# Kernel optimization log

Hardware: AMD Instinct MI355X
Metric: run time of the kernel (lower is better)

Reference implementation:

```python
import jax, jax.numpy as jnp
import numpy as np

N = 192            # image grid size (NxN)
N_SHOTS = 192
N_SAMPLES = 192
TWO_PI = 2.0 * np.pi
PIPE_ITERS = 3     # gpunufft default is ~10; 3 suffices for a CPU-runnable reference


def initialize_2D_radial(n_shots, n_samples):
    """Radial trajectory, k in [-0.5, 0.5), shape (n_shots*n_samples, 2)."""
    angles = np.pi * np.arange(n_shots) / n_shots
    radii = np.linspace(-0.5, 0.5, n_samples, endpoint=False)
    kx = radii[None, :] * np.cos(angles[:, None])
    ky = radii[None, :] * np.sin(angles[:, None])
    return np.stack([kx, ky], axis=-1).reshape(-1, 2).astype(np.float32)


def setup_inputs() -> dict:
    key = jax.random.key(0)
    x = jax.random.normal(key, (2, N, N), dtype=jnp.float32)  # real/imag image
    trajectory = jnp.asarray(initialize_2D_radial(N_SHOTS, N_SAMPLES))  # (M,2)
    return {"x": x, "trajectory": trajectory}


def _mats(traj):
    # Separable NDFT factors: exp(-2pi i k_x * px), exp(-2pi i k_y * py).
    # A: (M, N), B: (M, N); M*N complex64 ~= 57 MB each.
    p = jnp.arange(N, dtype=jnp.float32) - N / 2.0  # centered pixel coords
    A = jnp.exp(-1j * TWO_PI * traj[:, 0:1] * p[None, :])
    B = jnp.exp(-1j * TWO_PI * traj[:, 1:2] * p[None, :])
    return A.astype(jnp.complex64), B.astype(jnp.complex64)


def _op(img, A, B):
    # type-2 NUFFT (exact NDFT): image (N,N) -> kspace (M,)
    t = jnp.einsum('my,xy->mx', B, img)      # contract y first
    return jnp.einsum('mx,mx->m', A, t)


def _adj(d, A, B):
    # type-1 NUFFT adjoint: samples (M,) -> image (N,N)
    return jnp.einsum('mx,my->xy', jnp.conj(A) * d[:, None], jnp.conj(B))


def _pipe_density(A, B):
    # Pipe & Menon iterative density compensation: w <- w / |F F^H w|
    w = jnp.ones(A.shape[0], dtype=jnp.complex64)
    def body(i, w):
        q = _op(_adj(w, A, B), A, B)
        return w / jnp.maximum(jnp.abs(q), 1e-20)
    w = jax.lax.fori_loop(0, PIPE_ITERS, body, w)
    return jnp.abs(w)  # real positive weights


def reference(x, trajectory):
    img = (x[0] + 1j * x[1]).astype(jnp.complex64)  # (N,N) complex image
    A, B = _mats(trajectory)
    # density weights computed from detached trajectory (gpunufft init-time)
    traj_sg = jax.lax.stop_gradient(trajectory)
    Asg, Bsg = _mats(traj_sg)
    w = jax.lax.stop_gradient(_pipe_density(Asg, Bsg))
    kspace = _op(img, A, B)                       # forward NUFFT
    adjoint = _adj(w * kspace, A, B)              # density-compensated adjoint
    return jnp.stack([adjoint.real, adjoint.imag])  # (2,N,N) float32
```

## Files before the change

### kernel.cpp

```cpp
#include <hip/hip_runtime.h>
#include <math.h>


#define MTOT 36864
#define NPIX 192
#define SPLITS 128
#define MPS (MTOT / SPLITS)
#define ADJ_CHUNKS (MPS / 16)
#define PG 4

typedef __attribute__((ext_vector_type(8))) short s16x8;
typedef __attribute__((ext_vector_type(4))) float f32x4;
typedef __attribute__((ext_vector_type(4))) unsigned u32x4;

__device__ __forceinline__ f32x4 mfma_bf16(u32x4 a, u32x4 b, f32x4 c) {
    return __builtin_amdgcn_mfma_f32_16x16x32_bf16(
        __builtin_bit_cast(s16x8, a), __builtin_bit_cast(s16x8, b), c, 0, 0, 0);
}

__device__ __forceinline__ void g2l16(const void* g, void* l) {
    __builtin_amdgcn_global_load_lds(
        (const __attribute__((address_space(1))) void*)g,
        (__attribute__((address_space(3))) void*)l, 16, 0, 0);
}

__device__ __forceinline__ void split_pk(float a, float b, unsigned &hi, unsigned &lo) {
    const unsigned ua = __float_as_uint(a), ub = __float_as_uint(b);
    const unsigned ha = (ua + 0x8000u) & 0xffff0000u;
    const unsigned hb = (ub + 0x8000u) & 0xffff0000u;
    hi = (ha >> 16) | hb;
    const float la = a - __uint_as_float(ha);
    const float lb = b - __uint_as_float(hb);
    lo = ((__float_as_uint(la) + 0x8000u) >> 16) |
         ((__float_as_uint(lb) + 0x8000u) & 0xffff0000u);
}

__device__ __forceinline__ void ksplit(float k, float &kh, float &kl) {
    kh = __uint_as_float(__float_as_uint(k) & 0xfffff000u);
    kl = k - kh;
}
__device__ __forceinline__ float redphase(float kh, float kl, float p) {
    float r = kh * p;
    r -= rintf(r);
    r = fmaf(kl, p, r);
    return r;
}
__device__ __forceinline__ unsigned rot16(unsigned v) {
    return __builtin_amdgcn_alignbit(v, v, 16);
}
__device__ __forceinline__ int swz(int c) {
    return ((c ^ (c >> 2)) & 3) << 2;
}

__global__ void precompP_k(const float* __restrict__ traj, const int comp,
                           unsigned* __restrict__ PS) {
    const int m = blockIdx.x * 256 + threadIdx.x;
    const int c = blockIdx.y;
    float kh, kl; ksplit(traj[2 * m + comp], kh, kl);
    const float ph = redphase(kh, kl, (float)(c - 96));
    const float co = __builtin_amdgcn_cosf(ph);
    const float si = __builtin_amdgcn_sinf(ph);
    unsigned h, l; split_pk(co, -si, h, l);
    const int mc = m >> 4, mi = (m & 15) ^ swz(c);
    PS[(size_t)mc * 6144 + c * 16 + mi]        = h;
    PS[(size_t)mc * 6144 + 3072 + c * 16 + mi] = l;
}

__global__ void ebuild_k(const float* __restrict__ traj,
                         const float* __restrict__ dr, const float* __restrict__ di,
                         unsigned* __restrict__ ES) {
    const int m = blockIdx.x * 256 + threadIdx.x;
    const int c = blockIdx.y;
    float kh, kl; ksplit(traj[2 * m], kh, kl);
    const float ph = redphase(kh, kl, (float)(c - 96));
    const float co = __builtin_amdgcn_cosf(ph);
    const float si = __builtin_amdgcn_sinf(ph);
    const float dr_ = dr[m], di_ = di[m];
    const float Er = co * dr_ - si * di_;
    const float Ei = co * di_ + si * dr_;
    unsigned h, l; split_pk(Er, Ei, h, l);
    const int mc = m >> 4, mi = (m & 15) ^ swz(c);
    ES[(size_t)mc * 6144 + c * 16 + mi]        = h;
    ES[(size_t)mc * 6144 + 3072 + c * 16 + mi] = l;
}

__global__ void winit_k(float* __restrict__ wr, float* __restrict__ wi) {
    const int m = blockIdx.x * 256 + threadIdx.x;
    wr[m] = 1.f; wi[m] = 0.f;
}

__global__ __launch_bounds__(256) void adj_gemm_k(
    const unsigned* __restrict__ ES, const unsigned* __restrict__ BS,
    float* __restrict__ outP)
{
    __shared__ unsigned sAB[3][4096];
    const int tid = threadIdx.x;
    const int lane = tid & 63, wid = tid >> 6;
    const int l15 = lane & 15, qd = lane >> 4;
    const int L = blockIdx.x;
    const int xcd = L & 7, j = L >> 3;
    const int s = xcd * (SPLITS / 8) + j / 9;
    const int tile = j % 9;
    const int bx = tile % 3, by = tile / 3;
    const int wi = wid & 1, wj = wid >> 1;
    const int x0 = bx * 64 + wi * 32, y0 = by * 64 + wj * 32;
    float* outRe = outP + (size_t)(s & (PG - 1)) * (2 * MTOT);
    float* outIm = outRe + MTOT;

    f32x4 accRe[2][2], accIm[2][2];
    #pragma unroll
    for (int i = 0; i < 2; ++i)
        #pragma unroll
        for (int j2 = 0; j2 < 2; ++j2) {
            accRe[i][j2] = (f32x4){0.f, 0.f, 0.f, 0.f};
            accIm[i][j2] = (f32x4){0.f, 0.f, 0.f, 0.f};
        }

    const unsigned* gp[4];
    {
        const unsigned* E0 = ES + (size_t)(s * ADJ_CHUNKS) * 6144;
        const unsigned* B0 = BS + (size_t)(s * ADJ_CHUNKS) * 6144;
        gp[0] = E0 + bx * 1024 + tid * 4;
        gp[1] = E0 + 3072 + bx * 1024 + tid * 4;
        gp[2] = B0 + by * 1024 + tid * 4;
        gp[3] = B0 + 3072 + by * 1024 + tid * 4;
    }
    int eoff[2], boff[2];
    #pragma unroll
    for (int t = 0; t < 2; ++t) {
        const int cE = wi * 32 + t * 16 + l15;
        eoff[t] = cE * 16 + ((qd ^ ((cE ^ (cE >> 2)) & 3)) << 2);
        const int cB = wj * 32 + t * 16 + l15;
        boff[t] = 2048 + cB * 16 + ((qd ^ ((cB ^ (cB >> 2)) & 3)) << 2);
    }

    #pragma unroll
    for (int v = 0; v < 4; ++v)
        g2l16(gp[v], &sAB[0][v * 1024 + tid * 4]);
    #pragma unroll
    for (int v = 0; v < 4; ++v) {
        gp[v] += 6144;
        g2l16(gp[v], &sAB[1][v * 1024 + tid * 4]);
    }

    int rb = 0;
    for (int ch = 0; ch < ADJ_CHUNKS; ++ch) {
        if (ch + 2 < ADJ_CHUNKS) {
            const int wb = (rb + 2 >= 3) ? rb - 1 : rb + 2;
            #pragma unroll
            for (int v = 0; v < 4; ++v) {
                gp[v] += 6144;
                g2l16(gp[v], &sAB[wb][v * 1024 + tid * 4]);
            }
            asm volatile("s_waitcnt vmcnt(8)" ::: "memory");
        } else if (ch + 1 < ADJ_CHUNKS) {
            asm volatile("s_waitcnt vmcnt(4)" ::: "memory");
        } else {
            asm volatile("s_waitcnt vmcnt(0)" ::: "memory");
        }
        __builtin_amdgcn_s_barrier();

        const unsigned* sb = &sAB[rb][0];
        u32x4 Eh[2], El[2], PhA[2], PlA[2];
        #pragma unroll
        for (int t = 0; t < 2; ++t) {
            Eh[t]  = *(const u32x4*)(sb + eoff[t]);
            El[t]  = *(const u32x4*)(sb + 1024 + eoff[t]);
            PhA[t] = *(const u32x4*)(sb + boff[t]);
            PlA[t] = *(const u32x4*)(sb + 1024 + boff[t]);
        }
        asm volatile("s_waitcnt lgkmcnt(0)" ::: "memory");
        __builtin_amdgcn_sched_barrier(0);
        __builtin_amdgcn_s_barrier();

        #pragma unroll
        for (int sj = 0; sj < 2; ++sj) {
            const u32x4 Ph = PhA[sj], Pl = PlA[sj];
            u32x4 Qh, Ql;
            #pragma unroll
            for (int r = 0; r < 4; ++r) {
                Qh[r] = rot16(Ph[r]) ^ 0x00008000u;
                Ql[r] = rot16(Pl[r]) ^ 0x00008000u;
            }
            #pragma unroll
            for (int si = 0; si < 2; ++si) {
                accRe[si][sj] = mfma_bf16(Eh[si], Ph, accRe[si][sj]);
                accRe[si][sj] = mfma_bf16(Eh[si], Pl, accRe[si][sj]);
                accRe[si][sj] = mfma_bf16(El[si], Ph, accRe[si][sj]);
                accIm[si][sj] = mfma_bf16(Eh[si], Qh, accIm[si][sj]);
                accIm[si][sj] = mfma_bf16(Eh[si], Ql, accIm[si][sj]);
                accIm[si][sj] = mfma_bf16(El[si], Qh, accIm[si][sj]);
            }
        }
        rb = (rb + 1 == 3) ? 0 : rb + 1;
    }

    #pragma unroll
    for (int si = 0; si < 2; ++si)
        #pragma unroll
        for (int sj = 0; sj < 2; ++sj)
            #pragma unroll
            for (int rg = 0; rg < 4; ++rg) {
                const int x = x0 + si * 16 + qd * 4 + rg;
                const int y = y0 + sj * 16 + l15;
                atomicAdd(outRe + x * NPIX + y, accRe[si][sj][rg]);
                atomicAdd(outIm + x * NPIX + y, accIm[si][sj][rg]);
            }
}

__device__ __forceinline__ void fw_stage_load(const unsigned* __restrict__ Ghi,
                                              const unsigned* __restrict__ Glo,
                                              int tid, int koff, u32x4 st[3]) {
    #pragma unroll
    for (int j = 0; j < 3; ++j) {
        const int li = tid + j * 576;
        if (li < 1536) {
            const int row = li >> 3, pl = (li >> 2) & 1, qt = li & 3;
            const unsigned* src = pl ? Glo : Ghi;
            st[j] = *(const u32x4*)(src + row * 192 + koff + qt * 4);
        }
    }
}
__device__ __forceinline__ void fw_stage_write(unsigned* sb, int tid, const u32x4 st[3]) {
    #pragma unroll
    for (int j = 0; j < 3; ++j) {
        const int li = tid + j * 576;
        if (li < 1536) {
            const int row = li >> 3, pl = (li >> 2) & 1, qt = li & 3;
            *(u32x4*)(sb + pl * 3840 + row * 20 + qt * 4) = st[j];
        }
    }
}

__global__ __launch_bounds__(576) void fwdq_k(
    const float* __restrict__ traj,
    const unsigned* __restrict__ Ghi, const unsigned* __restrict__ Glo,
    float* __restrict__ wre, float* __restrict__ wim,
    const int mode,
    float* __restrict__ qre, float* __restrict__ qim)
{
    __shared__ unsigned sG[2][2 * 3840];
    const int tid = threadIdx.x;
    const int lane = tid & 63, wid = tid >> 6;
    const int l15 = lane & 15, q = lane >> 4;
    const int m = (blockIdx.x * 9 + wid) * 16 + l15;
    const float2 kk = *(const float2*)(traj + 2 * m);
    float kxh, kxl, kyh, kyl;
    ksplit(kk.x, kxh, kxl);
    ksplit(kk.y, kyh, kyl);

    f32x4 tre[12], tim[12];
    #pragma unroll
    for (int i = 0; i < 12; ++i) {
        tre[i] = (f32x4){0.f, 0.f, 0.f, 0.f};
        tim[i] = (f32x4){0.f, 0.f, 0.f, 0.f};
    }

    float bc, bs;
    { const float ph = redphase(kyh, kyl, (float)(q * 4 - 96)); 
      bc = __builtin_amdgcn_cosf(ph); bs = __builtin_amdgcn_sinf(ph); }
    const float r1c = __builtin_amdgcn_cosf(kk.y), r1s = __builtin_amdgcn_sinf(kk.y);
    float r16c, r16s;
    { float g = kk.y * 16.f; g -= rintf(g);
      r16c = __builtin_amdgcn_cosf(g); r16s = __builtin_amdgcn_sinf(g); }

    u32x4 st[3];
    fw_stage_load(Ghi, Glo, tid, 0, st);
    fw_stage_write(&sG[0][0], tid, st);
    __syncthreads();

    for (int ch = 0; ch < 12; ++ch) {
        if (ch < 11) fw_stage_load(Ghi, Glo, tid, (ch + 1) * 16, st);

        u32x4 Ph, Pl, Qh, Ql;
        {
            float c = bc, s = bs;
            #pragma unroll
            for (int r = 0; r < 4; ++r) {
                unsigned h, l; split_pk(c, s, h, l);
                Ph[r] = h; Pl[r] = l;
                Qh[r] = rot16(h) ^ 0x00008000u;
                Ql[r] = rot16(l) ^ 0x00008000u;
                const float nc = c * r1c - s * r1s, ns = s * r1c + c * r1s;
                c = nc; s = ns;
            }
            const float nbc = bc * r16c - bs * r16s, nbs = bs * r16c + bc * r16s;
            bc = nbc; bs = nbs;
        }

        const unsigned* sb = &sG[ch & 1][0];
        #pragma unroll
        for (int si = 0; si < 12; ++si) {
            const int base = (si * 16 + l15) * 20 + q * 4;
            const u32x4 gh = *(const u32x4*)(sb + base);
            const u32x4 gl = *(const u32x4*)(sb + 3840 + base);
            tre[si] = mfma_bf16(gh, Ph, tre[si]);
            tre[si] = mfma_bf16(gh, Pl, tre[si]);
            tre[si] = mfma_bf16(gl, Ph, tre[si]);
            tim[si] = mfma_bf16(gh, Qh, tim[si]);
            tim[si] = mfma_bf16(gh, Ql, tim[si]);
            tim[si] = mfma_bf16(gl, Qh, tim[si]);
        }

        if (ch < 11) {
            __syncthreads();
            fw_stage_write(&sG[(ch + 1) & 1][0], tid, st);
            __syncthreads();
        }
    }

    float qr = 0.f, qi = 0.f;
    {
        float g = kk.x * 16.f; g -= rintf(g);
        const float rc = __builtin_amdgcn_cosf(g), rs = __builtin_amdgcn_sinf(g);
        #pragma unroll
        for (int rg = 0; rg < 4; ++rg) {
            const float ph = redphase(kxh, kxl, (float)(q * 4 + rg - 96));
            float c = __builtin_amdgcn_cosf(ph), s = __builtin_amdgcn_sinf(ph);
            #pragma unroll
            for (int si = 0; si < 12; ++si) {
                const float tr = tre[si][rg], ti = tim[si][rg];
                qr += c * tr + s * ti;
                qi += c * ti - s * tr;
                const float nc = c * rc - s * rs, ns = s * rc + c * rs;
                c = nc; s = ns;
            }
        }
    }
    qr += __shfl_xor(qr, 16); qi += __shfl_xor(qi, 16);
    qr += __shfl_xor(qr, 32); qi += __shfl_xor(qi, 32);
    if (lane < 16) {
        if (mode == 0) {
            const float den = fmaxf(sqrtf(qr * qr + qi * qi), 1e-20f);
            wre[m] /= den; wim[m] /= den;
        } else {
            const float sc = sqrtf(wre[m] * wre[m] + wim[m] * wim[m]);
            qre[m] = qr * sc; qim[m] = qi * sc;
        }
    }
}

__global__ void presplit_k(const float* __restrict__ re, const float* __restrict__ im,
                           unsigned* __restrict__ Gh, unsigned* __restrict__ Gl) {
    const int e = blockIdx.x * 256 + threadIdx.x;
    unsigned h, l;
    split_pk(re[e], im[e], h, l);
    Gh[e] = h; Gl[e] = l;
}

__global__ void presplitP_k(const float* __restrict__ outP,
                            unsigned* __restrict__ Gh, unsigned* __restrict__ Gl) {
    const int e = blockIdx.x * 256 + threadIdx.x;
    float re = 0.f, im = 0.f;
    #pragma unroll
    for (int g = 0; g < PG; ++g) {
        re += outP[(size_t)g * (2 * MTOT) + e];
        im += outP[(size_t)g * (2 * MTOT) + MTOT + e];
    }
    unsigned h, l;
    split_pk(re, im, h, l);
    Gh[e] = h; Gl[e] = l;
}

__global__ void reduceOut_k(const float* __restrict__ outP, float* __restrict__ out) {
    const int e = blockIdx.x * 256 + threadIdx.x;
    float re = 0.f, im = 0.f;
    #pragma unroll
    for (int g = 0; g < PG; ++g) {
        re += outP[(size_t)g * (2 * MTOT) + e];
        im += outP[(size_t)g * (2 * MTOT) + MTOT + e];
    }
    out[e] = re; out[MTOT + e] = im;
}

extern "C" void kernel_launch(void* const* d_in, const int* in_sizes, int n_in,
                              void* d_out, int out_size, void* d_ws, size_t ws_size,
                              hipStream_t stream)
{
    const float* xin  = (const float*)d_in[0];
    const float* traj = (const float*)d_in[1];
    float* out = (float*)d_out;

    char* pb = (char*)d_ws;
    unsigned* BS = (unsigned*)pb; pb += (size_t)2304 * 6144 * 4;
    unsigned* ES = (unsigned*)pb; pb += (size_t)2304 * 6144 * 4;
    float* outP = (float*)pb; pb += (size_t)PG * 2 * MTOT * 4;
    float* wr   = (float*)pb; pb += MTOT * 4;
    float* wi   = (float*)pb; pb += MTOT * 4;
    float* dre  = (float*)pb; pb += MTOT * 4;
    float* dim_ = (float*)pb; pb += MTOT * 4;
    unsigned* Ghi = (unsigned*)pb; pb += MTOT * 4;
    unsigned* Glo = (unsigned*)pb; pb += MTOT * 4;

    precompP_k<<<dim3(MTOT / 256, NPIX), 256, 0, stream>>>(traj, 1, BS);
    winit_k<<<MTOT / 256, 256, 0, stream>>>(wr, wi);

    for (int it = 0; it < 3; ++it) {
        hipMemsetAsync(outP, 0, (size_t)PG * 2 * MTOT * 4, stream);
        ebuild_k<<<dim3(MTOT / 256, NPIX), 256, 0, stream>>>(traj, wr, wi, ES);
        adj_gemm_k<<<9 * SPLITS, 256, 0, stream>>>(ES, BS, outP);
        presplitP_k<<<MTOT / 256, 256, 0, stream>>>(outP, Ghi, Glo);
        fwdq_k<<<256, 576, 0, stream>>>(traj, Ghi, Glo, wr, wi, 0, dre, dim_);
    }

    presplit_k<<<MTOT / 256, 256, 0, stream>>>(xin, xin + MTOT, Ghi, Glo);
    fwdq_k<<<256, 576, 0, stream>>>(traj, Ghi, Glo, wr, wi, 1, dre, dim_);
    hipMemsetAsync(outP, 0, (size_t)PG * 2 * MTOT * 4, stream);
    ebuild_k<<<dim3(MTOT / 256, NPIX), 256, 0, stream>>>(traj, dre, dim_, ES);
    adj_gemm_k<<<9 * SPLITS, 256, 0, stream>>>(ES, BS, outP);
    reduceOut_k<<<MTOT / 256, 256, 0, stream>>>(outP, out);
}
```

Measured before the change: 497.9 us.

## Replace atomic split-K accumulation with per-group partial planes and drop memsets

```diff
diff --git a/kernel.cpp b/kernel.cpp
--- a/kernel.cpp
+++ b/kernel.cpp
@@ -5,9 +5,9 @@
 #define MTOT 36864
 #define NPIX 192
 #define SPLITS 128
-#define MPS (MTOT / SPLITS)
-#define ADJ_CHUNKS (MPS / 16)
-#define PG 4
+#define GRP 64
+#define NCH 36
+#define PG 64
 
 typedef __attribute__((ext_vector_type(8))) short s16x8;
 typedef __attribute__((ext_vector_type(4))) float f32x4;
@@ -99,12 +99,12 @@
     const int l15 = lane & 15, qd = lane >> 4;
     const int L = blockIdx.x;
     const int xcd = L & 7, j = L >> 3;
-    const int s = xcd * (SPLITS / 8) + j / 9;
+    const int g = xcd * (GRP / 8) + j / 9;
     const int tile = j % 9;
     const int bx = tile % 3, by = tile / 3;
     const int wi = wid & 1, wj = wid >> 1;
     const int x0 = bx * 64 + wi * 32, y0 = by * 64 + wj * 32;
-    float* outRe = outP + (size_t)(s & (PG - 1)) * (2 * MTOT);
+    float* outRe = outP + (size_t)g * (2 * MTOT);
     float* outIm = outRe + MTOT;
 
     f32x4 accRe[2][2], accIm[2][2];
@@ -116,15 +116,20 @@
             accIm[i][j2] = (f32x4){0.f, 0.f, 0.f, 0.f};
         }
 
-    const unsigned* gp[4];
-    {
-        const unsigned* E0 = ES + (size_t)(s * ADJ_CHUNKS) * 6144;
-        const unsigned* B0 = BS + (size_t)(s * ADJ_CHUNKS) * 6144;
-        gp[0] = E0 + bx * 1024 + tid * 4;
-        gp[1] = E0 + 3072 + bx * 1024 + tid * 4;
-        gp[2] = B0 + by * 1024 + tid * 4;
-        gp[3] = B0 + 3072 + by * 1024 + tid * 4;
-    }
+    const size_t g18 = (size_t)g * 18;
+    const int exo = bx * 1024 + tid * 4;
+    const int byo = by * 1024 + tid * 4;
+    #define STAGE(c, buf)                                                  \
+    {                                                                      \
+        const size_t id_ = (g18 + (c) + (((c) >= 18) ? 1134 : 0)) * 6144; \
+        const unsigned* E0_ = ES + id_;                                    \
+        const unsigned* B0_ = BS + id_;                                    \
+        g2l16(E0_ + exo,        &sAB[buf][tid * 4]);                       \
+        g2l16(E0_ + 3072 + exo, &sAB[buf][1024 + tid * 4]);                \
+        g2l16(B0_ + byo,        &sAB[buf][2048 + tid * 4]);                \
+        g2l16(B0_ + 3072 + byo, &sAB[buf][3072 + tid * 4]);                \
+    }
+
     int eoff[2], boff[2];
     #pragma unroll
     for (int t = 0; t < 2; ++t) {
@@ -134,26 +139,16 @@
         boff[t] = 2048 + cB * 16 + ((qd ^ ((cB ^ (cB >> 2)) & 3)) << 2);
     }
 
-    #pragma unroll
-    for (int v = 0; v < 4; ++v)
-        g2l16(gp[v], &sAB[0][v * 1024 + tid * 4]);
-    #pragma unroll
-    for (int v = 0; v < 4; ++v) {
-        gp[v] += 6144;
-        g2l16(gp[v], &sAB[1][v * 1024 + tid * 4]);
-    }
+    STAGE(0, 0);
+    STAGE(1, 1);
 
     int rb = 0;
-    for (int ch = 0; ch < ADJ_CHUNKS; ++ch) {
-        if (ch + 2 < ADJ_CHUNKS) {
+    for (int ch = 0; ch < NCH; ++ch) {
+        if (ch + 2 < NCH) {
             const int wb = (rb + 2 >= 3) ? rb - 1 : rb + 2;
-            #pragma unroll
-            for (int v = 0; v < 4; ++v) {
-                gp[v] += 6144;
-                g2l16(gp[v], &sAB[wb][v * 1024 + tid * 4]);
-            }
+            STAGE(ch + 2, wb);
             asm volatile("s_waitcnt vmcnt(8)" ::: "memory");
-        } else if (ch + 1 < ADJ_CHUNKS) {
+        } else if (ch + 1 < NCH) {
             asm volatile("s_waitcnt vmcnt(4)" ::: "memory");
         } else {
             asm volatile("s_waitcnt vmcnt(0)" ::: "memory");
@@ -194,6 +189,7 @@
         }
         rb = (rb + 1 == 3) ? 0 : rb + 1;
     }
+    #undef STAGE
 
     #pragma unroll
     for (int si = 0; si < 2; ++si)
@@ -203,8 +199,8 @@
             for (int rg = 0; rg < 4; ++rg) {
                 const int x = x0 + si * 16 + qd * 4 + rg;
                 const int y = y0 + sj * 16 + l15;
-                atomicAdd(outRe + x * NPIX + y, accRe[si][sj][rg]);
-                atomicAdd(outIm + x * NPIX + y, accIm[si][sj][rg]);
+                outRe[x * NPIX + y] = accRe[si][sj][rg];
+                outIm[x * NPIX + y] = accIm[si][sj][rg];
             }
 }
 
@@ -352,7 +348,7 @@
                             unsigned* __restrict__ Gh, unsigned* __restrict__ Gl) {
     const int e = blockIdx.x * 256 + threadIdx.x;
     float re = 0.f, im = 0.f;
-    #pragma unroll
+    #pragma unroll 8
     for (int g = 0; g < PG; ++g) {
         re += outP[(size_t)g * (2 * MTOT) + e];
         im += outP[(size_t)g * (2 * MTOT) + MTOT + e];
@@ -365,7 +361,7 @@
 __global__ void reduceOut_k(const float* __restrict__ outP, float* __restrict__ out) {
     const int e = blockIdx.x * 256 + threadIdx.x;
     float re = 0.f, im = 0.f;
-    #pragma unroll
+    #pragma unroll 8
     for (int g = 0; g < PG; ++g) {
         re += outP[(size_t)g * (2 * MTOT) + e];
         im += outP[(size_t)g * (2 * MTOT) + MTOT + e];
@@ -396,17 +392,15 @@
     winit_k<<<MTOT / 256, 256, 0, stream>>>(wr, wi);
 
     for (int it = 0; it < 3; ++it) {
-        hipMemsetAsync(outP, 0, (size_t)PG * 2 * MTOT * 4, stream);
         ebuild_k<<<dim3(MTOT / 256, NPIX), 256, 0, stream>>>(traj, wr, wi, ES);
-        adj_gemm_k<<<9 * SPLITS, 256, 0, stream>>>(ES, BS, outP);
+        adj_gemm_k<<<9 * GRP, 256, 0, stream>>>(ES, BS, outP);
         presplitP_k<<<MTOT / 256, 256, 0, stream>>>(outP, Ghi, Glo);
         fwdq_k<<<256, 576, 0, stream>>>(traj, Ghi, Glo, wr, wi, 0, dre, dim_);
     }
 
     presplit_k<<<MTOT / 256, 256, 0, stream>>>(xin, xin + MTOT, Ghi, Glo);
     fwdq_k<<<256, 576, 0, stream>>>(traj, Ghi, Glo, wr, wi, 1, dre, dim_);
-    hipMemsetAsync(outP, 0, (size_t)PG * 2 * MTOT * 4, stream);
     ebuild_k<<<dim3(MTOT / 256, NPIX), 256, 0, stream>>>(traj, dre, dim_, ES);
-    adj_gemm_k<<<9 * SPLITS, 256, 0, stream>>>(ES, BS, outP);
+    adj_gemm_k<<<9 * GRP, 256, 0, stream>>>(ES, BS, outP);
     reduceOut_k<<<MTOT / 256, 256, 0, stream>>>(outP, out);
 }
```

Result: faster. 463.2 us (-7.0%).
